# Optimization experiments

Measured on AMD Instinct MI355X. Metric: run time of the kernel, lower is better.

The kernel has to match this reference:

```python
import jax, jax.numpy as jnp
import numpy as np

DIM = 512
HEADS = 8
DH = 64
INNER = HEADS * DH  # 512
GRID = 32
FH, FW = GRID, GRID // 2 + 1


def _group_norm1(x, g, b, eps=1e-5):
    # GroupNorm(1, C) on NHWC: normalize over (H, W, C) per sample, per-channel affine
    mu = jnp.mean(x, axis=(1, 2, 3), keepdims=True)
    var = jnp.var(x, axis=(1, 2, 3), keepdims=True)
    return (x - mu) * jax.lax.rsqrt(var + eps) * g + b


def setup_inputs() -> dict:
    key = jax.random.key(0)
    ks = jax.random.split(key, 12)
    B, N, C = 8, GRID * GRID + 1, DIM
    s = 0.02
    return {
        "x": jax.random.normal(ks[0], (B, N, C), jnp.float32),
        "Wq": jax.random.normal(ks[1], (C, INNER), jnp.float32) * s,
        "Wk": jax.random.normal(ks[2], (C, INNER), jnp.float32) * s,
        "Wv": jax.random.normal(ks[3], (C, INNER), jnp.float32) * s,
        "dw_w": jax.random.normal(ks[4], (3, 3, 1, C), jnp.float32) * s,   # depthwise, HWIO
        "pw_w": jax.random.normal(ks[5], (C, INNER), jnp.float32) * s,     # 1x1 conv
        "ln_g": jnp.ones((INNER,), jnp.float32),
        "ln_b": jnp.zeros((INNER,), jnp.float32),
        "fr_wr": jnp.ones((FH, FW, C), jnp.float32),    # learnable FFT filter (real)
        "fr_wi": jnp.zeros((FH, FW, C), jnp.float32),   # learnable FFT filter (imag)
        "fr_pw": jax.random.normal(ks[6], (C, INNER), jnp.float32) * s,
        "fr_g": jnp.ones((INNER,), jnp.float32),
        "fr_b": jnp.zeros((INNER,), jnp.float32),
        "g_W1": jax.random.normal(ks[7], (3 * INNER, 3 * INNER // 4), jnp.float32) * s,
        "g_b1": jnp.zeros((3 * INNER // 4,), jnp.float32),
        "g_W2": jax.random.normal(ks[8], (3 * INNER // 4, 3), jnp.float32) * s,
        "g_b2": jnp.zeros((3,), jnp.float32),
        "Wp": jax.random.normal(ks[9], (INNER, DIM), jnp.float32) * s,
        "bp": jnp.zeros((DIM,), jnp.float32),
        "h_feat": GRID,
        "w_feat": GRID,
    }


def reference(x, Wq, Wk, Wv, dw_w, pw_w, ln_g, ln_b, fr_wr, fr_wi, fr_pw, fr_g, fr_b,
              g_W1, g_b1, g_W2, g_b2, Wp, bp, h_feat, w_feat):
    B, N, C = x.shape
    scale = DH ** -0.5
    has_cls = (N == h_feat * w_feat + 1)
    spatial = x[:, 1:] if has_cls else x

    # Branch 1: global self-attention (manual softmax attention)
    q = (x @ Wq).reshape(B, N, HEADS, DH)
    k = (x @ Wk).reshape(B, N, HEADS, DH)
    v = (x @ Wv).reshape(B, N, HEADS, DH)
    attn = jax.nn.softmax(jnp.einsum('bihd,bjhd->bhij', q, k) * scale, axis=-1)
    glob = jnp.einsum('bhij,bjhd->bihd', attn, v).reshape(B, N, INNER)

    # Branch 2: local depthwise conv -> pointwise conv -> GroupNorm(1)
    sp = spatial.reshape(B, h_feat, w_feat, C)  # NHWC
    dw = jax.lax.conv_general_dilated(sp, dw_w, (1, 1), 'SAME',
                                      dimension_numbers=('NHWC', 'HWIO', 'NHWC'),
                                      feature_group_count=C)
    loc = _group_norm1(jnp.einsum('bhwc,co->bhwo', dw, pw_w), ln_g, ln_b)
    loc = loc.reshape(B, h_feat * w_feat, INNER)
    if has_cls:
        loc = jnp.concatenate([loc.mean(axis=1, keepdims=True), loc], axis=1)

    # Branch 3: frequency enhancement (rfft2 -> learnable complex filter -> irfft2)
    xf = jnp.fft.rfft2(sp, axes=(1, 2), norm='ortho')               # (B, FH, FW, C)
    xf = xf * jax.lax.complex(fr_wr, fr_wi)[None]
    xe = jnp.fft.irfft2(xf, s=(h_feat, w_feat), axes=(1, 2), norm='ortho')
    fr = jax.nn.gelu(_group_norm1(jnp.einsum('bhwc,co->bhwo', xe, fr_pw), fr_g, fr_b),
                     approximate=False)
    fr = fr.reshape(B, h_feat * w_feat, INNER)
    if has_cls:
        fr = jnp.concatenate([fr.mean(axis=1, keepdims=True), fr], axis=1)

    # Gate MLP + softmax fusion
    cat = jnp.concatenate([glob, loc, fr], axis=-1)                  # (B, N, 3*INNER)
    gw = jax.nn.softmax(jax.nn.gelu(cat @ g_W1 + g_b1, approximate=False) @ g_W2 + g_b2,
                        axis=-1)                                     # (B, N, 3)
    fused = gw[..., 0:1] * glob + gw[..., 1:2] * loc + gw[..., 2:3] * fr
    return fused @ Wp + bp
```

## Files before the change

kernel.cpp:

```cpp
#include <hip/hip_runtime.h>
#include <math.h>

#define BB 8
#define NT 1025
#define CD 512
#define NH 8
#define DHD 64
#define HW 1024
#define FWD 17
#define MTOK 8200
#define MPAD 8320
#define QKS 1536

typedef __attribute__((ext_vector_type(8))) short short8;
typedef __attribute__((ext_vector_type(4))) float f32x4;
typedef __attribute__((ext_vector_type(16))) float f32x16;
typedef __attribute__((ext_vector_type(4))) unsigned u32x4;

__device__ __forceinline__ float gelu_exact(float x){
  return 0.5f * x * (1.0f + erff(x * 0.70710678118654752f));
}

__device__ __forceinline__ short f2bf(float f){
  unsigned u = __float_as_uint(f);
  unsigned r = (u + 0x7FFFu + ((u >> 16) & 1u)) >> 16;
  return (short)r;
}

__device__ __forceinline__ float bf2f(short s){
  unsigned u = ((unsigned)(unsigned short)s) << 16;
  return __uint_as_float(u);
}

__device__ __forceinline__ unsigned cvt_pk_bf16(float lo, float hi){
  unsigned r;
  asm volatile("v_cvt_pk_bf16_f32 %0, %1, %2" : "=v"(r) : "v"(lo), "v"(hi));
  return r;
}

__device__ __forceinline__ int xcd_logical(int phys, int n){
  int xcd = phys & 7, slot = phys >> 3;
  int q = n >> 3, r = n & 7;
  return xcd*q + (xcd < r ? xcd : r) + slot;
}

__global__ __launch_bounds__(256) void prep_all(
    const float* __restrict__ Wq, const float* __restrict__ Wk, const float* __restrict__ Wv,
    const float* __restrict__ pw, const float* __restrict__ frpw,
    const float* __restrict__ gW1, const float* __restrict__ Wp,
    short* __restrict__ wqkvt, short* __restrict__ pwt, short* __restrict__ frpwt,
    short* __restrict__ gw1t, short* __restrict__ wpt,
    const float* __restrict__ x, short* __restrict__ xb, float* __restrict__ stats)
{
  const int t = blockIdx.x;
  if (t >= 4192){
    int i0 = (t - 4192)*1024 + threadIdx.x;
    #pragma unroll
    for (int j = 0; j < 4; j++){
      int i = i0 + j*256;
      if (i < 8256) stats[i] = 0.f;
    }
    return;
  }
  if (t >= 2112){
    size_t i = ((size_t)(t - 2112)*256 + threadIdx.x) * 8;
    if (i >= (size_t)MPAD*CD) return;
    size_t row = i >> 9;
    short8 o;
    if (row < MTOK){
      #pragma unroll
      for (int j = 0; j < 8; j++) o[j] = f2bf(x[i+j]);
    } else {
      #pragma unroll
      for (int j = 0; j < 8; j++) o[j] = 0;
    }
    *(short8*)(xb + i) = o;
    return;
  }
  const float* W; short* Wt; int K, N, idx; float scale = 1.0f;
  if      (t < 256) { W = Wq;   Wt = wqkvt;            K=512;  N=512; idx=t;       scale=0.125f; }
  else if (t < 512) { W = Wk;   Wt = wqkvt+512*512;    K=512;  N=512; idx=t-256; }
  else if (t < 768) { W = Wv;   Wt = wqkvt+1024*512;   K=512;  N=512; idx=t-512; }
  else if (t < 1024){ W = pw;   Wt = pwt;              K=512;  N=512; idx=t-768; }
  else if (t < 1280){ W = frpw; Wt = frpwt;            K=512;  N=512; idx=t-1024; }
  else if (t < 1856){ W = gW1;  Wt = gw1t;             K=1536; N=384; idx=t-1280; }
  else              { W = Wp;   Wt = wpt;              K=512;  N=512; idx=t-1856; }
  const int ntn = N >> 5;
  const int n0 = (idx % ntn) << 5, k0 = (idx / ntn) << 5;
  __shared__ float tl[32][33];
  const int tx = threadIdx.x & 31, ty = threadIdx.x >> 5;
  #pragma unroll
  for (int i = 0; i < 32; i += 8)
    tl[ty+i][tx] = W[(size_t)(k0+ty+i)*N + n0+tx];
  __syncthreads();
  #pragma unroll
  for (int i = 0; i < 32; i += 8)
    Wt[(size_t)(n0+ty+i)*K + k0+tx] = f2bf(tl[tx][ty+i] * scale);
}

#define GEMM_DECL                                                          \
  __shared__ short As[128*64];                                             \
  __shared__ short Bs[64*64];                                              \
  const int tid = threadIdx.x;                                             \
  const int lane = tid & 63, wv = tid >> 6;                                \
  const int lc = lane & 15, lg = lane >> 4;                                \
  f32x4 acc[2][4];                                                         \
  _Pragma("unroll")                                                        \
  for (int rt=0;rt<2;rt++)                                                 \
    _Pragma("unroll")                                                      \
    for (int ct=0;ct<4;ct++) acc[rt][ct] = (f32x4){0.f,0.f,0.f,0.f};

#define GEMM_STAGE(Aptr, Ka, k0a, Bptr, Kb, k0b)                           \
  __syncthreads();                                                         \
  _Pragma("unroll")                                                        \
  for (int p = 0; p < 4; p++){                                             \
    int c = tid + p*256;                                                   \
    int r = c >> 3, s = c & 7;                                             \
    short8 v = *(const short8*)((Aptr) + (size_t)(row0 + r)*(Ka) + (k0a) + s*8); \
    *(short8*)&As[r*64 + ((s ^ (r & 7))*8)] = v;                           \
  }                                                                        \
  _Pragma("unroll")                                                        \
  for (int p = 0; p < 2; p++){                                             \
    int c = tid + p*256;                                                   \
    int r = c >> 3, s = c & 7;                                             \
    short8 v = *(const short8*)((Bptr) + (size_t)(col0 + r)*(Kb) + (k0b) + s*8); \
    *(short8*)&Bs[r*64 + ((s ^ (r & 7))*8)] = v;                           \
  }                                                                        \
  __syncthreads();

#define GEMM_COMPUTE                                                       \
  _Pragma("unroll")                                                        \
  for (int ks = 0; ks < 2; ks++){                                          \
    short8 af[2], bfr[4];                                                  \
    _Pragma("unroll")                                                      \
    for (int rt = 0; rt < 2; rt++){                                        \
      int r = wv*32 + rt*16 + lc;                                          \
      af[rt] = *(const short8*)&As[r*64 + (((ks*4+lg) ^ (r & 7))*8)];      \
    }                                                                      \
    _Pragma("unroll")                                                      \
    for (int ct = 0; ct < 4; ct++){                                        \
      int r = ct*16 + lc;                                                  \
      bfr[ct] = *(const short8*)&Bs[r*64 + (((ks*4+lg) ^ (r & 7))*8)];     \
    }                                                                      \
    _Pragma("unroll")                                                      \
    for (int rt = 0; rt < 2; rt++)                                         \
      _Pragma("unroll")                                                    \
      for (int ct = 0; ct < 4; ct++)                                       \
        acc[rt][ct] = __builtin_amdgcn_mfma_f32_16x16x32_bf16(af[rt], bfr[ct], acc[rt][ct], 0,0,0); \
  }

__global__ __launch_bounds__(256) void gemm_mega(
    const short* __restrict__ xb, const short* __restrict__ wqkvt, short* __restrict__ qkvb,
    const short* __restrict__ aL, const short* __restrict__ bL, short* __restrict__ cL,
    float* __restrict__ totL,
    const short* __restrict__ aF, const short* __restrict__ bF, short* __restrict__ cF,
    float* __restrict__ totF)
{
  const int l = xcd_logical(blockIdx.x, 2584);
  const short *A, *Bt; short* Cm; float* tot = nullptr;
  int N, row0, col0;
  if (l < 1560){
    A = xb; Bt = wqkvt; Cm = qkvb; N = 1536;
    row0 = (l / 24) * 128; col0 = (l % 24) * 64;
  } else if (l < 2072){
    int l2 = l - 1560;
    A = aL; Bt = bL; Cm = cL; tot = totL; N = 512;
    row0 = (l2 >> 3) * 128; col0 = (l2 & 7) * 64;
  } else {
    int l2 = l - 2072;
    A = aF; Bt = bF; Cm = cF; tot = totF; N = 512;
    row0 = (l2 >> 3) * 128; col0 = (l2 & 7) * 64;
  }
  const int K = 512;
  GEMM_DECL;
  for (int k0 = 0; k0 < K; k0 += 64){
    GEMM_STAGE(A, K, k0, Bt, K, k0);
    GEMM_COMPUTE;
  }
  float s1 = 0.f, s2 = 0.f;
  #pragma unroll
  for (int rt = 0; rt < 2; rt++)
    #pragma unroll
    for (int e = 0; e < 4; e++){
      int gr = row0 + wv*32 + rt*16 + lg*4 + e;
      #pragma unroll
      for (int ct = 0; ct < 4; ct++){
        int gc = col0 + ct*16 + lc;
        float v = acc[rt][ct][e];
        Cm[(size_t)gr*N + gc] = f2bf(v);
        s1 += v; s2 += v*v;
      }
    }
  if (tot){
    #pragma unroll
    for (int o = 32; o > 0; o >>= 1){ s1 += __shfl_xor(s1, o); s2 += __shfl_xor(s2, o); }
    if (lane == 0){
      atomicAdd(&tot[(row0>>10)*2],   s1);
      atomicAdd(&tot[(row0>>10)*2+1], s2);
    }
  }
}

__global__ __launch_bounds__(256) void gemm_final(
    const short* __restrict__ A, const short* __restrict__ Bt,
    const float* __restrict__ bias, float* __restrict__ Cm, int M)
{
  const int N = 512, K = 512;
  const int l = xcd_logical(blockIdx.x, gridDim.x);
  const int row0 = (l >> 3) * 128, col0 = (l & 7) * 64;
  GEMM_DECL;
  for (int k0 = 0; k0 < K; k0 += 64){
    GEMM_STAGE(A, K, k0, Bt, K, k0);
    GEMM_COMPUTE;
  }
  #pragma unroll
  for (int rt = 0; rt < 2; rt++)
    #pragma unroll
    for (int e = 0; e < 4; e++){
      int gr = row0 + wv*32 + rt*16 + lg*4 + e;
      if (gr >= M) continue;
      #pragma unroll
      for (int ct = 0; ct < 4; ct++){
        int gc = col0 + ct*16 + lc;
        Cm[(size_t)gr*N + gc] = acc[rt][ct][e] + bias[gc];
      }
    }
}

__global__ __launch_bounds__(256) void gemm_gate(
    const short* __restrict__ A0, const short* __restrict__ A1, const short* __restrict__ A2,
    const short* __restrict__ Bt, const float* __restrict__ bias, short* __restrict__ Cm,
    int M)
{
  const int N = 384, K = 1536;
  const int l = xcd_logical(blockIdx.x, gridDim.x);
  const int row0 = (l / 6) * 128, col0 = (l % 6) * 64;
  GEMM_DECL;
  for (int kt = 0; kt < 24; kt++){
    int k0 = kt * 64;
    const short* Asrc = (k0 < 512) ? A0 : (k0 < 1024 ? A1 : A2);
    const int kb = k0 & 511;
    GEMM_STAGE(Asrc, 512, kb, Bt, K, k0);
    GEMM_COMPUTE;
  }
  #pragma unroll
  for (int rt = 0; rt < 2; rt++)
    #pragma unroll
    for (int e = 0; e < 4; e++){
      int gr = row0 + wv*32 + rt*16 + lg*4 + e;
      if (gr >= M) continue;
      #pragma unroll
      for (int ct = 0; ct < 4; ct++){
        int gc = col0 + ct*16 + lc;
        float v = acc[rt][ct][e] + bias[gc];
        Cm[(size_t)gr*N + gc] = f2bf(gelu_exact(v));
      }
    }
}

__global__ __launch_bounds__(256) void attn_mfma32(
    const short* __restrict__ qkv, short* __restrict__ glob)
{
  const int bi = blockIdx.x;
  const int xcd = bi & 7;
  const int jj = bi >> 3;
  const int gq = jj / 9;
  const int qt = jj - gq*9;
  const int g  = xcd + 8*gq;
  const int h  = g & 7, b = g >> 3;

  const int tid = threadIdx.x;
  const int lane = tid & 63, wq = tid >> 6;
  const int q32 = lane & 31;
  const int hi  = lane >> 5;
  const int bN = b * NT;
  const int q0w = qt*128 + wq*32;

  __shared__ short Kl[2][64*64];
  __shared__ short Vl[2][64*64];

  short8 qf[4];
  {
    int qr = q0w + q32; if (qr > 1024) qr = 1024;
    const short* qp = qkv + (size_t)(bN + qr)*QKS + h*DHD + hi*8;
    qf[0] = *(const short8*)(qp);
    qf[1] = *(const short8*)(qp + 16);
    qf[2] = *(const short8*)(qp + 32);
    qf[3] = *(const short8*)(qp + 48);
  }

  f32x16 oA = {0.f,0.f,0.f,0.f,0.f,0.f,0.f,0.f,0.f,0.f,0.f,0.f,0.f,0.f,0.f,0.f};
  f32x16 oB = oA;
  float rs = 0.f;

  const int kc0 = tid;
  const int kc1 = tid + 256;
  const int vkey = tid & 63, vdg = tid >> 6;
  const short* kgbase = qkv + (size_t)bN*QKS + 512 + h*DHD;
  const short* vgbase = qkv + (size_t)bN*QKS + 1024 + h*DHD;

  short8 gk0, gk1, gv0, gv1;
  auto loadT = [&](int kt2){
    gk0 = *(const short8*)(kgbase + (size_t)(kt2*64 + (kc0>>3))*QKS + (kc0&7)*8);
    gk1 = *(const short8*)(kgbase + (size_t)(kt2*64 + (kc1>>3))*QKS + (kc1&7)*8);
    gv0 = *(const short8*)(vgbase + (size_t)(kt2*64 + vkey)*QKS + vdg*16);
    gv1 = *(const short8*)(vgbase + (size_t)(kt2*64 + vkey)*QKS + vdg*16 + 8);
  };
  auto writeT = [&](int buf){
    { int r = kc0>>3, sl = kc0&7;
      *(short8*)&Kl[buf][r*64 + (((sl) ^ (r&7))*8)] = gk0; }
    { int r = kc1>>3, sl = kc1&7;
      *(short8*)&Kl[buf][r*64 + (((sl) ^ (r&7))*8)] = gk1; }
    #pragma unroll
    for (int i2 = 0; i2 < 8; i2++){
      int d0 = vdg*16 + i2, d1 = vdg*16 + 8 + i2;
      Vl[buf][d0*64 + (((vkey>>3) ^ (d0&7))*8) + (vkey&7)] = gv0[i2];
      Vl[buf][d1*64 + (((vkey>>3) ^ (d1&7))*8) + (vkey&7)] = gv1[i2];
    }
  };

  loadT(0);
  writeT(0);
  __syncthreads();

  for (int kt = 0; kt < 17; kt++){
    const int cur = kt & 1;
    if (kt < 16) loadT(kt+1);

    #pragma unroll
    for (int ks = 0; ks < 2; ks++){
      f32x16 s = {0.f,0.f,0.f,0.f,0.f,0.f,0.f,0.f,0.f,0.f,0.f,0.f,0.f,0.f,0.f,0.f};
      const int krow = ks*32 + q32;
      const int kbase = krow*64;
      const int kx = q32 & 7;
      __builtin_amdgcn_s_setprio(1);
      #pragma unroll
      for (int kk = 0; kk < 4; kk++){
        short8 af = *(const short8*)&Kl[cur][kbase + (((2*kk+hi) ^ kx)*8)];
        s = __builtin_amdgcn_mfma_f32_32x32x16_bf16(af, qf[kk], s, 0,0,0);
      }
      __builtin_amdgcn_s_setprio(0);
      float p[16];
      if (kt == 16){
        #pragma unroll
        for (int e = 0; e < 16; e++){
          bool valid = (ks == 0) && (e == 0) && (hi == 0);
          p[e] = valid ? __expf(s[e]) : 0.f;
        }
      } else {
        #pragma unroll
        for (int e = 0; e < 16; e++) p[e] = __expf(s[e]);
      }
      #pragma unroll
      for (int e = 0; e < 16; e++) rs += p[e];
      unsigned pk[4][2];
      #pragma unroll
      for (int g2 = 0; g2 < 4; g2++){
        pk[g2][0] = cvt_pk_bf16(p[4*g2+0], p[4*g2+1]);
        pk[g2][1] = cvt_pk_bf16(p[4*g2+2], p[4*g2+3]);
      }
      #pragma unroll
      for (int kc = 0; kc < 2; kc++){
        unsigned e00 = pk[2*kc][0],   e01 = pk[2*kc][1];
        unsigned e10 = pk[2*kc+1][0], e11 = pk[2*kc+1][1];
        unsigned t00 = (unsigned)__shfl_xor((int)e00, 32);
        unsigned t01 = (unsigned)__shfl_xor((int)e01, 32);
        unsigned t10 = (unsigned)__shfl_xor((int)e10, 32);
        unsigned t11 = (unsigned)__shfl_xor((int)e11, 32);
        u32x4 pu;
        pu[0] = hi ? t10 : e00;
        pu[1] = hi ? t11 : e01;
        pu[2] = hi ? e10 : t00;
        pu[3] = hi ? e11 : t01;
        short8 pa = *(short8*)&pu;
        const int vsl = 4*ks + 2*kc + hi;
        __builtin_amdgcn_s_setprio(1);
        {
          short8 vf0 = *(const short8*)&Vl[cur][(q32)*64      + ((vsl ^ kx)*8)];
          oA = __builtin_amdgcn_mfma_f32_32x32x16_bf16(pa, vf0, oA, 0,0,0);
          short8 vf1 = *(const short8*)&Vl[cur][(32+q32)*64   + ((vsl ^ kx)*8)];
          oB = __builtin_amdgcn_mfma_f32_32x32x16_bf16(pa, vf1, oB, 0,0,0);
        }
        __builtin_amdgcn_s_setprio(0);
      }
    }

    if (kt < 16){
      writeT(cur ^ 1);
      __syncthreads();
    }
  }

  float rs_tot = rs + __shfl_xor(rs, 32);
  #pragma unroll
  for (int e = 0; e < 16; e++){
    int rowr = (e & 3) + 8*(e >> 2) + 4*hi;
    int q = q0w + rowr;
    if (q > 1024) continue;
    float inv = 1.0f / __shfl(rs_tot, rowr);
    size_t base = (size_t)(bN + q)*CD + h*DHD + q32;
    glob[base]      = f2bf(oA[e] * inv);
    glob[base + 32] = f2bf(oB[e] * inv);
  }
}

__global__ __launch_bounds__(512) void dwconv(
    const short* __restrict__ xb, const float* __restrict__ w, short* __restrict__ out)
{
  const int c = threadIdx.x;
  const int xx = blockIdx.x & 31;
  const int yg = (blockIdx.x >> 5) & 7;
  const int b  = blockIdx.x >> 8;
  const int y0 = yg << 2;
  float acc[4] = {0.f,0.f,0.f,0.f};
  #pragma unroll
  for (int dx = -1; dx <= 1; dx++){
    int x2 = xx + dx;
    if (x2 < 0 || x2 > 31) continue;
    float col[6];
    #pragma unroll
    for (int r = 0; r < 6; r++){
      int row = y0 - 1 + r;
      col[r] = (row >= 0 && row < 32)
             ? bf2f(xb[((size_t)(b*NT + 1 + row*32 + x2))*CD + c]) : 0.f;
    }
    float w0 = w[(0*3+dx+1)*CD + c];
    float w1 = w[(1*3+dx+1)*CD + c];
    float w2 = w[(2*3+dx+1)*CD + c];
    #pragma unroll
    for (int o = 0; o < 4; o++)
      acc[o] += col[o]*w0 + col[o+1]*w1 + col[o+2]*w2;
  }
  #pragma unroll
  for (int o = 0; o < 4; o++)
    out[((size_t)(b*HW + (y0+o)*32 + xx))*CD + c] = f2bf(acc[o]);
}

__global__ __launch_bounds__(512) void gn_apply2(
    const short* __restrict__ mmL, const short* __restrict__ mmF,
    const float* __restrict__ totL, const float* __restrict__ totF,
    const float* __restrict__ gL, const float* __restrict__ bL,
    const float* __restrict__ gF, const float* __restrict__ bF,
    short* __restrict__ loc, short* __restrict__ fr,
    float* __restrict__ colsumL, float* __restrict__ colsumF)
{
  const int br = blockIdx.x >> 8;
  const int bi = blockIdx.x & 255;
  const int c = threadIdx.x;
  const int b = bi >> 5;
  const int p0 = (bi & 31) << 5;
  const short* mm = br ? mmF : mmL;
  const float* tot = br ? totF : totL;
  short* out = br ? fr : loc;
  float* colsum = br ? colsumF : colsumL;
  const float inv = 1.0f / ((float)HW * CD);
  const float mu = tot[b*2] * inv;
  const float rstd = rsqrtf(tot[b*2+1]*inv - mu*mu + 1e-5f);
  const float gc = (br ? gF : gL)[c], bc = (br ? bF : bL)[c];
  float s = 0.0f;
  for (int r = 0; r < 32; r++){
    int p = p0 + r;
    float v = bf2f(mm[((size_t)b*HW + p)*CD + c]);
    v = (v - mu) * rstd * gc + bc;
    if (br) v = gelu_exact(v);
    out[((size_t)(b*NT + 1 + p))*CD + c] = f2bf(v);
    s += v;
  }
  atomicAdd(&colsum[b*CD + c], s);
}

__global__ __launch_bounds__(512) void colmean_fin2(
    const float* __restrict__ colsumL, const float* __restrict__ colsumF,
    short* __restrict__ loc, short* __restrict__ fr)
{
  const int c = threadIdx.x;
  const int b = blockIdx.x & 7;
  if (blockIdx.x < 8) loc[((size_t)b*NT)*CD + c] = f2bf(colsumL[b*CD + c] * (1.0f/HW));
  else                fr [((size_t)b*NT)*CD + c] = f2bf(colsumF[b*CD + c] * (1.0f/HW));
}

__global__ __launch_bounds__(512) void fft_f1(
    const float* __restrict__ x, float* __restrict__ Ur, float* __restrict__ Ui)
{
  const int c = threadIdx.x;
  const int xx = blockIdx.x & 31;
  const int b = blockIdx.x >> 5;
  __shared__ float ct[32], st[32];
  if (c < 32){ float ang = 6.283185307179586f * c / 32.0f; ct[c] = cosf(ang); st[c] = sinf(ang); }
  __syncthreads();
  float v[32];
  #pragma unroll
  for (int y = 0; y < 32; y++) v[y] = x[((size_t)(b*NT + 1 + y*32 + xx))*CD + c];
  for (int ky = 0; ky <= 16; ky++){
    float sr = 0.f, si = 0.f;
    #pragma unroll
    for (int y = 0; y < 32; y++){
      int idx = (ky*y) & 31;
      sr += v[y]*ct[idx]; si -= v[y]*st[idx];
    }
    size_t o = ((size_t)((b*17+ky)*32+xx))*CD + c;
    Ur[o] = sr; Ui[o] = si;
  }
}

__global__ __launch_bounds__(256) void fft_f2(
    const float* __restrict__ Ur, const float* __restrict__ Ui,
    const float* __restrict__ wr, const float* __restrict__ wi,
    float* __restrict__ Gr, float* __restrict__ Gi)
{
  const int c = (blockIdx.x & 1)*256 + threadIdx.x;
  const int t = blockIdx.x >> 1;
  const int ky = t % 17, b = t / 17;
  __shared__ float ct[32], st[32];
  if (threadIdx.x < 32){ float ang = 6.283185307179586f * threadIdx.x / 32.0f;
    ct[threadIdx.x] = cosf(ang); st[threadIdx.x] = sinf(ang); }
  __syncthreads();
  float ar[32], ai[32];
  #pragma unroll
  for (int kx = 0; kx < 32; kx++){ ar[kx] = 0.f; ai[kx] = 0.f; }
  #pragma unroll
  for (int xx = 0; xx < 32; xx++){
    size_t o = ((size_t)((b*17+ky)*32+xx))*CD + c;
    float ur = Ur[o], ui = Ui[o];
    #pragma unroll
    for (int kx = 0; kx < 32; kx++){
      int idx = (kx*xx) & 31;
      float cc = ct[idx], ss = st[idx];
      ar[kx] += ur*cc + ui*ss;
      ai[kx] += ui*cc - ur*ss;
    }
  }
  #pragma unroll
  for (int kx = 0; kx < FWD; kx++){
    size_t fo = ((size_t)(ky*FWD+kx))*CD + c;
    float fwr = wr[fo], fwi = wi[fo];
    size_t go = ((size_t)((b*17+kx)*32+ky))*CD + c;
    Gr[go] = ar[kx]*fwr - ai[kx]*fwi;
    Gi[go] = ar[kx]*fwi + ai[kx]*fwr;
  }
  if (ky >= 1 && ky <= 15){
    const int ky2 = 32 - ky;
    #pragma unroll
    for (int kx = 0; kx < FWD; kx++){
      int m = (32 - kx) & 31;
      size_t fo = ((size_t)(ky2*FWD+kx))*CD + c;
      float fwr = wr[fo], fwi = wi[fo];
      size_t go = ((size_t)((b*17+kx)*32+ky2))*CD + c;
      Gr[go] = ar[m]*fwr + ai[m]*fwi;
      Gi[go] = ar[m]*fwi - ai[m]*fwr;
    }
  }
}

__global__ __launch_bounds__(256) void fft_f3(
    const float* __restrict__ Gr, const float* __restrict__ Gi,
    float* __restrict__ Tr, float* __restrict__ Ti)
{
  const int c = (blockIdx.x & 1)*256 + threadIdx.x;
  const int t = blockIdx.x >> 1;
  const int kx = t % 17, b = t / 17;
  __shared__ float ct[32], st[32];
  if (threadIdx.x < 32){ float ang = 6.283185307179586f * threadIdx.x / 32.0f;
    ct[threadIdx.x] = cosf(ang); st[threadIdx.x] = sinf(ang); }
  __syncthreads();
  float tr[32], ti[32];
  #pragma unroll
  for (int y = 0; y < 32; y++){ tr[y] = 0.f; ti[y] = 0.f; }
  #pragma unroll
  for (int ky = 0; ky < 32; ky++){
    size_t go = ((size_t)((b*17+kx)*32+ky))*CD + c;
    float gr = Gr[go], gi = Gi[go];
    #pragma unroll
    for (int y = 0; y < 32; y++){
      int idx = (ky*y) & 31;
      float cc = ct[idx], ss = st[idx];
      tr[y] += gr*cc - gi*ss;
      ti[y] += gr*ss + gi*cc;
    }
  }
  #pragma unroll
  for (int y = 0; y < 32; y++){
    size_t to = ((size_t)((b*32+y)*17+kx))*CD + c;
    Tr[to] = tr[y]*(1.0f/32.0f);
    Ti[to] = ti[y]*(1.0f/32.0f);
  }
}

__global__ __launch_bounds__(512) void fft_f4(
    const float* __restrict__ Tr, const float* __restrict__ Ti, short* __restrict__ xe)
{
  const int c = threadIdx.x;
  const int y = blockIdx.x & 31;
  const int b = blockIdx.x >> 5;
  __shared__ float ct[32], st[32];
  if (c < 32){ float ang = 6.283185307179586f * c / 32.0f; ct[c] = cosf(ang); st[c] = sinf(ang); }
  __syncthreads();
  float tr[FWD], ti[FWD];
  #pragma unroll
  for (int kx = 0; kx < FWD; kx++){
    size_t o = ((size_t)((b*32+y)*17+kx))*CD + c;
    tr[kx] = Tr[o]; ti[kx] = Ti[o];
  }
  for (int x2 = 0; x2 < 32; x2++){
    float acc = tr[0] + ((x2 & 1) ? -tr[16] : tr[16]);
    #pragma unroll
    for (int k2 = 1; k2 < 16; k2++){
      int idx = (k2*x2) & 31;
      acc += 2.0f*(tr[k2]*ct[idx] - ti[k2]*st[idx]);
    }
    xe[((size_t)(b*HW + y*32 + x2))*CD + c] = f2bf(acc*(1.0f/32.0f));
  }
}

__global__ __launch_bounds__(256) void gate_fuse(
    const short* __restrict__ h1, const float* __restrict__ gW2, const float* __restrict__ gb2,
    const short* __restrict__ glob, const short* __restrict__ loc, const short* __restrict__ fr,
    short* __restrict__ fused)
{
  const int token = blockIdx.x*4 + (threadIdx.x >> 6);
  const int lane = threadIdx.x & 63;
  if (token >= MTOK) return;
  float p0 = 0.f, p1 = 0.f, p2 = 0.f;
  #pragma unroll
  for (int i = 0; i < 6; i++){
    int idx = lane + i*64;
    float h = bf2f(h1[(size_t)token*384 + idx]);
    p0 += h * gW2[idx*3+0]; p1 += h * gW2[idx*3+1]; p2 += h * gW2[idx*3+2];
  }
  #pragma unroll
  for (int o = 32; o > 0; o >>= 1){
    p0 += __shfl_xor(p0, o); p1 += __shfl_xor(p1, o); p2 += __shfl_xor(p2, o);
  }
  p0 += gb2[0]; p1 += gb2[1]; p2 += gb2[2];
  float mx = fmaxf(p0, fmaxf(p1, p2));
  float e0 = __expf(p0-mx), e1 = __expf(p1-mx), e2 = __expf(p2-mx);
  float inv = 1.0f/(e0+e1+e2);
  float g0 = e0*inv, g1 = e1*inv, g2 = e2*inv;
  #pragma unroll
  for (int i = 0; i < 8; i++){
    size_t o2 = (size_t)token*CD + lane + i*64;
    fused[o2] = f2bf(g0*bf2f(glob[o2]) + g1*bf2f(loc[o2]) + g2*bf2f(fr[o2]));
  }
}

extern "C" void kernel_launch(void* const* d_in, const int* in_sizes, int n_in,
                              void* d_out, int out_size, void* d_ws, size_t ws_size,
                              hipStream_t stream)
{
  const float* x     = (const float*)d_in[0];
  const float* Wq    = (const float*)d_in[1];
  const float* Wk    = (const float*)d_in[2];
  const float* Wv    = (const float*)d_in[3];
  const float* dw_w  = (const float*)d_in[4];
  const float* pw_w  = (const float*)d_in[5];
  const float* ln_g  = (const float*)d_in[6];
  const float* ln_b  = (const float*)d_in[7];
  const float* fr_wr = (const float*)d_in[8];
  const float* fr_wi = (const float*)d_in[9];
  const float* fr_pw = (const float*)d_in[10];
  const float* fr_g  = (const float*)d_in[11];
  const float* fr_b  = (const float*)d_in[12];
  const float* g_W1  = (const float*)d_in[13];
  const float* g_b1  = (const float*)d_in[14];
  const float* g_W2  = (const float*)d_in[15];
  const float* g_b2  = (const float*)d_in[16];
  const float* Wp    = (const float*)d_in[17];
  const float* bp    = (const float*)d_in[18];

  float* ws = (float*)d_ws;
  float* scrA = ws;
  float* scrB = scrA + 8388608;
  float* stats = scrB + 4456448;
  float* totL    = stats;
  float* totF    = stats + 16;
  float* colsumL = stats + 64;
  float* colsumF = stats + 64 + 4096;

  const size_t RPAD = 8448;
  short* glob  = (short*)(stats + 16384);
  short* loc   = glob  + RPAD*CD;
  short* fr    = loc   + RPAD*CD;
  short* actbL = fr    + RPAD*CD;
  short* actbF = actbL + RPAD*CD;
  short* fused = actbL;
  short* qkvb  = actbF + RPAD*CD;
  short* xb    = qkvb + (size_t)MPAD*QKS;
  short* wqkvt = xb + (size_t)MPAD*CD;
  short* pwt   = wqkvt + 1536*512;
  short* frpwt = pwt + 512*512;
  short* gw1t  = frpwt + 512*512;
  short* wpt   = gw1t + 384*1536;
  short* mmL = (short*)scrA;
  short* mmF = mmL + (size_t)8192*CD;

  prep_all<<<4201, 256, 0, stream>>>(Wq, Wk, Wv, pw_w, fr_pw, g_W1, Wp,
                                     wqkvt, pwt, frpwt, gw1t, wpt, x, xb, stats);

  dwconv<<<BB*8*32, 512, 0, stream>>>(xb, dw_w, actbL);
  float* Ur = scrA;            float* Ui = scrA + 2228224;
  float* Gr = scrB;            float* Gi = scrB + 2228224;
  float* Tr = scrA;            float* Ti = scrA + 2228224;
  fft_f1<<<BB*32, 512, 0, stream>>>(x, Ur, Ui);
  fft_f2<<<BB*17*2, 256, 0, stream>>>(Ur, Ui, fr_wr, fr_wi, Gr, Gi);
  fft_f3<<<BB*17*2, 256, 0, stream>>>(Gr, Gi, Tr, Ti);
  fft_f4<<<BB*32, 512, 0, stream>>>(Tr, Ti, actbF);

  gemm_mega<<<2584, 256, 0, stream>>>(xb, wqkvt, qkvb,
                                      actbL, pwt, mmL, totL,
                                      actbF, frpwt, mmF, totF);

  attn_mfma32<<<576, 256, 0, stream>>>(qkvb, glob);

  gn_apply2<<<512, 512, 0, stream>>>(mmL, mmF, totL, totF, ln_g, ln_b, fr_g, fr_b,
                                     loc, fr, colsumL, colsumF);
  colmean_fin2<<<16, 512, 0, stream>>>(colsumL, colsumF, loc, fr);

  gemm_gate<<<390, 256, 0, stream>>>(glob, loc, fr, gw1t, g_b1, (short*)scrB, MTOK);
  gate_fuse<<<2050, 256, 0, stream>>>((short*)scrB, g_W2, g_b2, glob, loc, fr, fused);
  gemm_final<<<520, 256, 0, stream>>>(fused, wpt, bp, (float*)d_out, MTOK);
}
```

Measured before the change: 307.3 us.

## Widen mega-GEMM tiles to 128x128 and merge independent kernels into combined launches

The QKV/pointwise mega-GEMM now uses 128x128 output tiles instead of 128x64, which halves the block count and lets each A tile feed twice as many MFMAs. Depthwise conv and the first FFT stage are merged into one launch, and attention and GroupNorm-apply are merged into another, with blocks dispatched by index range. The merges are meant to cut launch overhead and let independent work overlap on the device. The wider tile raises accumulator register use and may lower occupancy, and the GN blocks share a kernel with attention's LDS allocation.

```diff
diff --git a/kernel.cpp b/kernel.cpp
--- a/kernel.cpp
+++ b/kernel.cpp
@@ -156,27 +156,72 @@
     const short* __restrict__ aF, const short* __restrict__ bF, short* __restrict__ cF,
     float* __restrict__ totF)
 {
-  const int l = xcd_logical(blockIdx.x, 2584);
+  const int l = xcd_logical(blockIdx.x, 1292);
   const short *A, *Bt; short* Cm; float* tot = nullptr;
   int N, row0, col0;
-  if (l < 1560){
+  if (l < 780){
     A = xb; Bt = wqkvt; Cm = qkvb; N = 1536;
-    row0 = (l / 24) * 128; col0 = (l % 24) * 64;
-  } else if (l < 2072){
-    int l2 = l - 1560;
+    row0 = (l / 12) * 128; col0 = (l % 12) * 128;
+  } else if (l < 1036){
+    int l2 = l - 780;
     A = aL; Bt = bL; Cm = cL; tot = totL; N = 512;
-    row0 = (l2 >> 3) * 128; col0 = (l2 & 7) * 64;
+    row0 = (l2 >> 2) * 128; col0 = (l2 & 3) * 128;
   } else {
-    int l2 = l - 2072;
+    int l2 = l - 1036;
     A = aF; Bt = bF; Cm = cF; tot = totF; N = 512;
-    row0 = (l2 >> 3) * 128; col0 = (l2 & 7) * 64;
+    row0 = (l2 >> 2) * 128; col0 = (l2 & 3) * 128;
   }
   const int K = 512;
-  GEMM_DECL;
+
+  __shared__ short As[128*64];
+  __shared__ short Bs[128*64];
+  const int tid = threadIdx.x;
+  const int lane = tid & 63, wv = tid >> 6;
+  const int lc = lane & 15, lg = lane >> 4;
+  f32x4 acc[2][8];
+  #pragma unroll
+  for (int rt=0;rt<2;rt++)
+    #pragma unroll
+    for (int ct=0;ct<8;ct++) acc[rt][ct] = (f32x4){0.f,0.f,0.f,0.f};
+
   for (int k0 = 0; k0 < K; k0 += 64){
-    GEMM_STAGE(A, K, k0, Bt, K, k0);
-    GEMM_COMPUTE;
-  }
+    __syncthreads();
+    #pragma unroll
+    for (int p = 0; p < 4; p++){
+      int c = tid + p*256;
+      int r = c >> 3, s = c & 7;
+      short8 v = *(const short8*)(A + (size_t)(row0 + r)*K + k0 + s*8);
+      *(short8*)&As[r*64 + ((s ^ (r & 7))*8)] = v;
+    }
+    #pragma unroll
+    for (int p = 0; p < 4; p++){
+      int c = tid + p*256;
+      int r = c >> 3, s = c & 7;
+      short8 v = *(const short8*)(Bt + (size_t)(col0 + r)*K + k0 + s*8);
+      *(short8*)&Bs[r*64 + ((s ^ (r & 7))*8)] = v;
+    }
+    __syncthreads();
+    #pragma unroll
+    for (int ks = 0; ks < 2; ks++){
+      short8 af[2], bfr[8];
+      #pragma unroll
+      for (int rt = 0; rt < 2; rt++){
+        int r = wv*32 + rt*16 + lc;
+        af[rt] = *(const short8*)&As[r*64 + (((ks*4+lg) ^ (r & 7))*8)];
+      }
+      #pragma unroll
+      for (int ct = 0; ct < 8; ct++){
+        int r = ct*16 + lc;
+        bfr[ct] = *(const short8*)&Bs[r*64 + (((ks*4+lg) ^ (r & 7))*8)];
+      }
+      #pragma unroll
+      for (int rt = 0; rt < 2; rt++)
+        #pragma unroll
+        for (int ct = 0; ct < 8; ct++)
+          acc[rt][ct] = __builtin_amdgcn_mfma_f32_16x16x32_bf16(af[rt], bfr[ct], acc[rt][ct], 0,0,0);
+    }
+  }
+
   float s1 = 0.f, s2 = 0.f;
   #pragma unroll
   for (int rt = 0; rt < 2; rt++)
@@ -184,7 +229,7 @@
     for (int e = 0; e < 4; e++){
       int gr = row0 + wv*32 + rt*16 + lg*4 + e;
       #pragma unroll
-      for (int ct = 0; ct < 4; ct++){
+      for (int ct = 0; ct < 8; ct++){
         int gc = col0 + ct*16 + lc;
         float v = acc[rt][ct][e];
         Cm[(size_t)gr*N + gc] = f2bf(v);
@@ -258,9 +303,47 @@
     }
 }
 
-__global__ __launch_bounds__(256) void attn_mfma32(
-    const short* __restrict__ qkv, short* __restrict__ glob)
-{
+__global__ __launch_bounds__(256) void attn_gn(
+    const short* __restrict__ qkv, short* __restrict__ glob,
+    const short* __restrict__ mmL, const short* __restrict__ mmF,
+    const float* __restrict__ totL, const float* __restrict__ totF,
+    const float* __restrict__ gL, const float* __restrict__ bL,
+    const float* __restrict__ gF, const float* __restrict__ bF,
+    short* __restrict__ loc, short* __restrict__ fr,
+    float* __restrict__ colsumL, float* __restrict__ colsumF)
+{
+  __shared__ short Kl[2][64*64];
+  __shared__ short Vl[2][64*64];
+
+  if (blockIdx.x >= 576){
+    const int bi2 = blockIdx.x - 576;
+    const int br = bi2 >> 9;
+    const int rem = bi2 & 511;
+    const int b = rem >> 6;
+    const int sub = rem & 63;
+    const int p0 = (sub >> 1) << 5;
+    const int c = (sub & 1)*256 + threadIdx.x;
+    const short* mm = br ? mmF : mmL;
+    const float* tot = br ? totF : totL;
+    short* out = br ? fr : loc;
+    float* colsum = br ? colsumF : colsumL;
+    const float inv = 1.0f / ((float)HW * CD);
+    const float mu = tot[b*2] * inv;
+    const float rstd = rsqrtf(tot[b*2+1]*inv - mu*mu + 1e-5f);
+    const float gc = (br ? gF : gL)[c], bc = (br ? bF : bL)[c];
+    float s = 0.0f;
+    for (int r = 0; r < 32; r++){
+      int p = p0 + r;
+      float v = bf2f(mm[((size_t)b*HW + p)*CD + c]);
+      v = (v - mu) * rstd * gc + bc;
+      if (br) v = gelu_exact(v);
+      out[((size_t)(b*NT + 1 + p))*CD + c] = f2bf(v);
+      s += v;
+    }
+    atomicAdd(&colsum[b*CD + c], s);
+    return;
+  }
+
   const int bi = blockIdx.x;
   const int xcd = bi & 7;
   const int jj = bi >> 3;
@@ -275,9 +358,6 @@
   const int hi  = lane >> 5;
   const int bN = b * NT;
   const int q0w = qt*128 + wq*32;
-
-  __shared__ short Kl[2][64*64];
-  __shared__ short Vl[2][64*64];
 
   short8 qf[4];
   {
@@ -404,9 +484,33 @@
   }
 }
 
-__global__ __launch_bounds__(512) void dwconv(
-    const short* __restrict__ xb, const float* __restrict__ w, short* __restrict__ out)
-{
+__global__ __launch_bounds__(512) void dw_fft1(
+    const short* __restrict__ xb, const float* __restrict__ w, short* __restrict__ out,
+    const float* __restrict__ x, float* __restrict__ Ur, float* __restrict__ Ui)
+{
+  __shared__ float ct[32], st[32];
+  if (blockIdx.x >= 2048){
+    const int bi = blockIdx.x - 2048;
+    const int c = threadIdx.x;
+    const int xx = bi & 31;
+    const int b = bi >> 5;
+    if (c < 32){ float ang = 6.283185307179586f * c / 32.0f; ct[c] = cosf(ang); st[c] = sinf(ang); }
+    __syncthreads();
+    float v[32];
+    #pragma unroll
+    for (int y = 0; y < 32; y++) v[y] = x[((size_t)(b*NT + 1 + y*32 + xx))*CD + c];
+    for (int ky = 0; ky <= 16; ky++){
+      float sr = 0.f, si = 0.f;
+      #pragma unroll
+      for (int y = 0; y < 32; y++){
+        int idx = (ky*y) & 31;
+        sr += v[y]*ct[idx]; si -= v[y]*st[idx];
+      }
+      size_t o = ((size_t)((b*17+ky)*32+xx))*CD + c;
+      Ur[o] = sr; Ui[o] = si;
+    }
+    return;
+  }
   const int c = threadIdx.x;
   const int xx = blockIdx.x & 31;
   const int yg = (blockIdx.x >> 5) & 7;
@@ -436,39 +540,6 @@
     out[((size_t)(b*HW + (y0+o)*32 + xx))*CD + c] = f2bf(acc[o]);
 }
 
-__global__ __launch_bounds__(512) void gn_apply2(
-    const short* __restrict__ mmL, const short* __restrict__ mmF,
-    const float* __restrict__ totL, const float* __restrict__ totF,
-    const float* __restrict__ gL, const float* __restrict__ bL,
-    const float* __restrict__ gF, const float* __restrict__ bF,
-    short* __restrict__ loc, short* __restrict__ fr,
-    float* __restrict__ colsumL, float* __restrict__ colsumF)
-{
-  const int br = blockIdx.x >> 8;
-  const int bi = blockIdx.x & 255;
-  const int c = threadIdx.x;
-  const int b = bi >> 5;
-  const int p0 = (bi & 31) << 5;
-  const short* mm = br ? mmF : mmL;
-  const float* tot = br ? totF : totL;
-  short* out = br ? fr : loc;
-  float* colsum = br ? colsumF : colsumL;
-  const float inv = 1.0f / ((float)HW * CD);
-  const float mu = tot[b*2] * inv;
-  const float rstd = rsqrtf(tot[b*2+1]*inv - mu*mu + 1e-5f);
-  const float gc = (br ? gF : gL)[c], bc = (br ? bF : bL)[c];
-  float s = 0.0f;
-  for (int r = 0; r < 32; r++){
-    int p = p0 + r;
-    float v = bf2f(mm[((size_t)b*HW + p)*CD + c]);
-    v = (v - mu) * rstd * gc + bc;
-    if (br) v = gelu_exact(v);
-    out[((size_t)(b*NT + 1 + p))*CD + c] = f2bf(v);
-    s += v;
-  }
-  atomicAdd(&colsum[b*CD + c], s);
-}
-
 __global__ __launch_bounds__(512) void colmean_fin2(
     const float* __restrict__ colsumL, const float* __restrict__ colsumF,
     short* __restrict__ loc, short* __restrict__ fr)
@@ -477,30 +548,6 @@
   const int b = blockIdx.x & 7;
   if (blockIdx.x < 8) loc[((size_t)b*NT)*CD + c] = f2bf(colsumL[b*CD + c] * (1.0f/HW));
   else                fr [((size_t)b*NT)*CD + c] = f2bf(colsumF[b*CD + c] * (1.0f/HW));
-}
-
-__global__ __launch_bounds__(512) void fft_f1(
-    const float* __restrict__ x, float* __restrict__ Ur, float* __restrict__ Ui)
-{
-  const int c = threadIdx.x;
-  const int xx = blockIdx.x & 31;
-  const int b = blockIdx.x >> 5;
-  __shared__ float ct[32], st[32];
-  if (c < 32){ float ang = 6.283185307179586f * c / 32.0f; ct[c] = cosf(ang); st[c] = sinf(ang); }
-  __syncthreads();
-  float v[32];
-  #pragma unroll
-  for (int y = 0; y < 32; y++) v[y] = x[((size_t)(b*NT + 1 + y*32 + xx))*CD + c];
-  for (int ky = 0; ky <= 16; ky++){
-    float sr = 0.f, si = 0.f;
-    #pragma unroll
-    for (int y = 0; y < 32; y++){
-      int idx = (ky*y) & 31;
-      sr += v[y]*ct[idx]; si -= v[y]*st[idx];
-    }
-    size_t o = ((size_t)((b*17+ky)*32+xx))*CD + c;
-    Ur[o] = sr; Ui[o] = si;
-  }
 }
 
 __global__ __launch_bounds__(256) void fft_f2(
@@ -696,23 +743,21 @@
   prep_all<<<4201, 256, 0, stream>>>(Wq, Wk, Wv, pw_w, fr_pw, g_W1, Wp,
                                      wqkvt, pwt, frpwt, gw1t, wpt, x, xb, stats);
 
-  dwconv<<<BB*8*32, 512, 0, stream>>>(xb, dw_w, actbL);
   float* Ur = scrA;            float* Ui = scrA + 2228224;
   float* Gr = scrB;            float* Gi = scrB + 2228224;
   float* Tr = scrA;            float* Ti = scrA + 2228224;
-  fft_f1<<<BB*32, 512, 0, stream>>>(x, Ur, Ui);
+  dw_fft1<<<2304, 512, 0, stream>>>(xb, dw_w, actbL, x, Ur, Ui);
   fft_f2<<<BB*17*2, 256, 0, stream>>>(Ur, Ui, fr_wr, fr_wi, Gr, Gi);
   fft_f3<<<BB*17*2, 256, 0, stream>>>(Gr, Gi, Tr, Ti);
   fft_f4<<<BB*32, 512, 0, stream>>>(Tr, Ti, actbF);
 
-  gemm_mega<<<2584, 256, 0, stream>>>(xb, wqkvt, qkvb,
+  gemm_mega<<<1292, 256, 0, stream>>>(xb, wqkvt, qkvb,
                                       actbL, pwt, mmL, totL,
                                       actbF, frpwt, mmF, totF);
 
-  attn_mfma32<<<576, 256, 0, stream>>>(qkvb, glob);
-
-  gn_apply2<<<512, 512, 0, stream>>>(mmL, mmF, totL, totF, ln_g, ln_b, fr_g, fr_b,
-                                     loc, fr, colsumL, colsumF);
+  attn_gn<<<1600, 256, 0, stream>>>(qkvb, glob, mmL, mmF, totL, totF,
+                                    ln_g, ln_b, fr_g, fr_b,
+                                    loc, fr, colsumL, colsumF);
   colmean_fin2<<<16, 512, 0, stream>>>(colsumL, colsumF, loc, fr);
 
   gemm_gate<<<390, 256, 0, stream>>>(glob, loc, fr, gw1t, g_b1, (short*)scrB, MTOK);
```

Result: faster. 266.0 us (-13.4%).
